# Kernel optimization log

Hardware: AMD Instinct MI355X
Metric: run time of the kernel (lower is better)

## Reference

```python
import jax, jax.numpy as jnp
import numpy as np

B, S, V, E, H, A, L = 64, 256, 32000, 512, 512, 512, 2
EPS = 1e-5


def _ln(x, g, b):
    m = jnp.mean(x, axis=-1, keepdims=True)
    v = jnp.mean((x - m) ** 2, axis=-1, keepdims=True)
    return (x - m) * jax.lax.rsqrt(v + EPS) * g + b


def _lstm_cell(x, h, c, W_ih, W_hh, b_ih, b_hh):
    # torch gate order: i, f, g, o
    gates = x @ W_ih.T + b_ih + h @ W_hh.T + b_hh  # [B, 4H]
    i, f, g, o = jnp.split(gates, 4, axis=-1)
    i, f, o = jax.nn.sigmoid(i), jax.nn.sigmoid(f), jax.nn.sigmoid(o)
    g = jnp.tanh(g)
    c_new = f * c + i * g
    h_new = o * jnp.tanh(c_new)
    return h_new, c_new


def setup_inputs() -> dict:
    key = jax.random.key(0)
    ks = jax.random.split(key, 24)
    d = {}
    d['input_token'] = jax.random.randint(ks[0], (B, 1), 0, V)
    d['h0'] = jax.random.normal(ks[1], (L, B, H), jnp.float32)
    d['c0'] = jax.random.normal(ks[2], (L, B, H), jnp.float32)
    d['encoder_outputs'] = jax.random.normal(ks[3], (B, S, 2 * H), jnp.float32)
    d['encoder_mask'] = jnp.ones((B, S), jnp.int32)
    sc = lambda fi, fo: float(np.sqrt(6.0 / (fi + fo)))
    d['emb'] = jax.random.normal(ks[4], (V, E), jnp.float32) * 0.1
    d['ln_emb_g'] = jnp.ones((E,), jnp.float32)
    d['ln_emb_b'] = jnp.zeros((E,), jnp.float32)
    d['W_enc'] = jax.random.uniform(ks[5], (A, 2 * H), jnp.float32, -sc(2 * H, A), sc(2 * H, A))
    d['b_enc'] = jnp.zeros((A,), jnp.float32)
    d['W_dec'] = jax.random.uniform(ks[6], (A, H), jnp.float32, -sc(H, A), sc(H, A))
    d['b_dec'] = jnp.zeros((A,), jnp.float32)
    d['v_att'] = jax.random.uniform(ks[7], (1, A), jnp.float32, -sc(A, 1), sc(A, 1))
    d['ln_att_g'] = jnp.ones((A,), jnp.float32)
    d['ln_att_b'] = jnp.zeros((A,), jnp.float32)
    in0, in1 = E + 2 * H, H
    d['W_ih0'] = jax.random.uniform(ks[8], (4 * H, in0), jnp.float32, -sc(in0, 4 * H), sc(in0, 4 * H))
    d['W_hh0'] = jax.random.normal(ks[9], (4 * H, H), jnp.float32) * 0.05
    d['b_ih0'] = jnp.zeros((4 * H,), jnp.float32).at[H:2 * H].set(1.0)
    d['b_hh0'] = jnp.zeros((4 * H,), jnp.float32)
    d['W_ih1'] = jax.random.uniform(ks[10], (4 * H, in1), jnp.float32, -sc(in1, 4 * H), sc(in1, 4 * H))
    d['W_hh1'] = jax.random.normal(ks[11], (4 * H, H), jnp.float32) * 0.05
    d['b_ih1'] = jnp.zeros((4 * H,), jnp.float32).at[H:2 * H].set(1.0)
    d['b_hh1'] = jnp.zeros((4 * H,), jnp.float32)
    d['ln_lstm_g'] = jnp.ones((H,), jnp.float32)
    d['ln_lstm_b'] = jnp.zeros((H,), jnp.float32)
    d['W_ctx'] = jax.random.uniform(ks[12], (H, 2 * H), jnp.float32, -sc(2 * H, H), sc(2 * H, H))
    d['b_ctx'] = jnp.zeros((H,), jnp.float32)
    d['W_out'] = jax.random.uniform(ks[13], (V, H), jnp.float32, -sc(H, V), sc(H, V))
    d['b_out'] = jnp.zeros((V,), jnp.float32)
    return d


def reference(input_token, h0, c0, encoder_outputs, encoder_mask,
              emb, ln_emb_g, ln_emb_b,
              W_enc, b_enc, W_dec, b_dec, v_att, ln_att_g, ln_att_b,
              W_ih0, W_hh0, b_ih0, b_hh0, W_ih1, W_hh1, b_ih1, b_hh1,
              ln_lstm_g, ln_lstm_b, W_ctx, b_ctx, W_out, b_out):
    # embedding + norm (dropout = identity in eval)
    embedded = _ln(emb[input_token], ln_emb_g, ln_emb_b)  # [B,1,E]

    # attention using top-layer hidden state
    dec_h = h0[-1]  # [B,H]
    enc_proj = jnp.einsum('bsk,ak->bsa', encoder_outputs, W_enc) + b_enc
    dec_proj = dec_h @ W_dec.T + b_dec  # [B,A]
    combined = _ln(enc_proj + dec_proj[:, None, :], ln_att_g, ln_att_b)
    scores = jnp.einsum('bsa,a->bs', jnp.tanh(combined), v_att[0])
    scores = jnp.where(encoder_mask == 0, -jnp.inf, scores)
    attn_w = jax.nn.softmax(scores, axis=1)  # [B,S]
    context = jnp.einsum('bs,bsk->bk', attn_w, encoder_outputs)  # [B,2H]

    # single-step 2-layer LSTM
    x = jnp.concatenate([embedded[:, 0, :], context], axis=-1)  # [B,E+2H]
    h_l0, c_l0 = _lstm_cell(x, h0[0], c0[0], W_ih0, W_hh0, b_ih0, b_hh0)
    h_l1, c_l1 = _lstm_cell(h_l0, h0[1], c0[1], W_ih1, W_hh1, b_ih1, b_hh1)
    h_new = jnp.stack([h_l0, h_l1])
    c_new = jnp.stack([c_l0, c_l1])

    lstm_out = _ln(h_l1, ln_lstm_g, ln_lstm_b)  # [B,H]
    proj_ctx = context @ W_ctx.T + b_ctx  # [B,H]
    logits = (lstm_out + proj_ctx) @ W_out.T + b_out  # [B,V]
    return logits[:, None, :], (h_new, c_new), attn_w
```

## Files before the change

### kernel.cpp

```cpp
#include <hip/hip_runtime.h>

typedef unsigned int u32;
typedef unsigned short u16;
typedef __attribute__((ext_vector_type(8))) short short8;
typedef __attribute__((ext_vector_type(4))) float f32x4;

__device__ __forceinline__ float bf2f(u16 u) {
  union { u32 i; float f; } v; v.i = ((u32)u) << 16; return v.f;
}
__device__ __forceinline__ u16 f2bf(float f) {
  union { float f; u32 i; } v; v.f = f;
  u32 u = v.i;
  u += 0x7FFFu + ((u >> 16) & 1u);
  return (u16)(u >> 16);
}
__device__ __forceinline__ float tanh_fast(float x) {
  float e = __expf(-2.f * fabsf(x));
  float r = (1.f - e) / (1.f + e);
  return x < 0.f ? -r : r;
}
__device__ __forceinline__ float sigmoid_fast(float x) {
  return 1.f / (1.f + __expf(-x));
}
__device__ __forceinline__ float ld1r(const void* p, size_t i, int f32w) {
  return f32w ? ((const float*)p)[i] : bf2f(((const u16*)p)[i]);
}
__device__ __forceinline__ void outst(void* p, size_t i, float v, int f32o) {
  if (f32o) ((float*)p)[i] = v; else ((u16*)p)[i] = f2bf(v);
}
__device__ __forceinline__ int flag_of(const u32* lnegp) {
  return (lnegp[0] == 0x3F800000u) ? 1 : 0;
}

#define OFF_H    2048000
#define OFF_C    2113536
#define OFF_ATTN 2179072

#define A_LNAG 0
#define A_LNAB 512
#define A_VAT  1024
#define A_BENC 1536
#define A_BDEC 2048
#define A_BIH0 2560
#define A_BHH0 4608
#define A_BIH1 6656
#define A_BHH1 8704
#define A_LNLG 10752
#define A_LNLB 11264
#define A_BCTX 11776
#define A_BOUT 12288
#define A_TOTAL 44288

struct SrcPtrs {
  const void *h0, *c0, *emb, *lneg, *lneb, *Wenc, *benc, *Wdec, *bdec, *vat,
             *lnag, *lnab, *bih0, *bhh0, *bih1, *bhh1, *lnlg, *lnlb, *Wctx,
             *bctx, *bout;
  const int *tok;
};

__device__ __forceinline__ void convblk_r(const void* src, u16* dst, size_t base, int f32w) {
  size_t i0 = base + (size_t)threadIdx.x * 16;
  if (f32w) {
    const float* s = (const float*)src + i0;
    float4 a = *(const float4*)s, b = *(const float4*)(s + 4);
    float4 c = *(const float4*)(s + 8), d = *(const float4*)(s + 12);
    short8 v0, v1;
    v0[0]=(short)f2bf(a.x); v0[1]=(short)f2bf(a.y); v0[2]=(short)f2bf(a.z); v0[3]=(short)f2bf(a.w);
    v0[4]=(short)f2bf(b.x); v0[5]=(short)f2bf(b.y); v0[6]=(short)f2bf(b.z); v0[7]=(short)f2bf(b.w);
    v1[0]=(short)f2bf(c.x); v1[1]=(short)f2bf(c.y); v1[2]=(short)f2bf(c.z); v1[3]=(short)f2bf(c.w);
    v1[4]=(short)f2bf(d.x); v1[5]=(short)f2bf(d.y); v1[6]=(short)f2bf(d.z); v1[7]=(short)f2bf(d.w);
    *(short8*)(dst + i0) = v0; *(short8*)(dst + i0 + 8) = v1;
  } else {
    const uint4* s = (const uint4*)((const u16*)src + i0);
    uint4 a = s[0], b = s[1];
    *(uint4*)(dst + i0) = a; *((uint4*)(dst + i0) + 1) = b;
  }
}

__global__ __launch_bounds__(256) void k_conv(
    const u32* __restrict__ lnegp, SrcPtrs P,
    u16* __restrict__ xcat, u16* __restrict__ xcat1,
    float* __restrict__ c0f, float* __restrict__ arena,
    u16* __restrict__ Wencbf, u16* __restrict__ Wctxbf,
    float* __restrict__ dpf)
{
  const int f32w = flag_of(lnegp);
  __shared__ float red[8];
  __shared__ float hs[512];
  __shared__ float part[256];
  const int t = threadIdx.x;
  const int blk = blockIdx.x;
  if (blk < 64) {
    const int b = blk;
    const int tk = P.tok[b];
    float e0 = ld1r(P.emb, (size_t)tk * 512 + t, f32w);
    float e1 = ld1r(P.emb, (size_t)tk * 512 + t + 256, f32w);
    float s = e0 + e1, ss = e0 * e0 + e1 * e1;
    #pragma unroll
    for (int o = 1; o < 64; o <<= 1) { s += __shfl_xor(s, o, 64); ss += __shfl_xor(ss, o, 64); }
    if ((t & 63) == 0) { red[t >> 6] = s; red[4 + (t >> 6)] = ss; }
    __syncthreads();
    s = red[0] + red[1] + red[2] + red[3];
    ss = red[4] + red[5] + red[6] + red[7];
    const float mean = s * (1.f / 512.f);
    const float rstd = rsqrtf(fmaxf(ss * (1.f / 512.f) - mean * mean, 0.f) + 1e-5f);
    xcat[b*2048 + t]       = f2bf((e0 - mean) * rstd * ld1r(P.lneg, t, f32w) + ld1r(P.lneb, t, f32w));
    xcat[b*2048 + t + 256] = f2bf((e1 - mean) * rstd * ld1r(P.lneg, t + 256, f32w) + ld1r(P.lneb, t + 256, f32w));
    xcat[b*2048 + 1536 + t]       = f2bf(ld1r(P.h0, (size_t)b * 512 + t, f32w));
    xcat[b*2048 + 1536 + t + 256] = f2bf(ld1r(P.h0, (size_t)b * 512 + t + 256, f32w));
  } else if (blk < 128) {
    const int b = blk - 64;
    for (int j = t; j < 512; j += 256) {
      float h1 = ld1r(P.h0, 32768 + (size_t)b * 512 + j, f32w);
      xcat1[b*1024 + 512 + j] = f2bf(h1);
      c0f[b*512 + j]         = ld1r(P.c0, (size_t)b * 512 + j, f32w);
      c0f[32768 + b*512 + j] = ld1r(P.c0, 32768 + (size_t)b * 512 + j, f32w);
    }
  } else if (blk < 256) {
    const int qb = (blk - 128) * 512;
    #pragma unroll
    for (int u = 0; u < 2; u++) {
      int Qi = qb + u * 256 + t;
      int kc = Qi >> 11, rem = Qi & 2047;
      int cq = rem >> 9, col = rem & 511;
      size_t src = (size_t)col * 1024 + kc * 32 + cq * 8;
      if (f32w) {
        const float* s = (const float*)P.Wenc + src;
        float4 a = *(const float4*)s, b2 = *(const float4*)(s + 4);
        short8 v;
        v[0]=(short)f2bf(a.x); v[1]=(short)f2bf(a.y); v[2]=(short)f2bf(a.z); v[3]=(short)f2bf(a.w);
        v[4]=(short)f2bf(b2.x); v[5]=(short)f2bf(b2.y); v[6]=(short)f2bf(b2.z); v[7]=(short)f2bf(b2.w);
        *(short8*)(Wencbf + (size_t)Qi * 8) = v;
      } else {
        *(uint4*)(Wencbf + (size_t)Qi * 8) = *(const uint4*)((const u16*)P.Wenc + src);
      }
    }
  } else if (blk < 384) {
    convblk_r(P.Wctx, Wctxbf, (size_t)(blk - 256) * 4096, f32w);
  } else if (blk < 640) {
    const int db = blk - 384;
    const int b2 = db >> 2, cg = db & 3;
    if (f32w) {
      float2 v = *(const float2*)((const float*)P.h0 + 32768 + (size_t)b2 * 512 + t * 2);
      hs[t * 2] = v.x; hs[t * 2 + 1] = v.y;
    } else {
      u32 u2 = *(const u32*)((const u16*)P.h0 + 32768 + (size_t)b2 * 512 + t * 2);
      hs[t * 2] = bf2f((u16)(u2 & 0xffff)); hs[t * 2 + 1] = bf2f((u16)(u2 >> 16));
    }
    __syncthreads();
    const int col = cg * 128 + (t & 127);
    const int kh = (t >> 7) * 256;
    float acc = 0.f;
    if (f32w) {
      const float* wp = (const float*)P.Wdec + (size_t)col * 512 + kh;
      #pragma unroll 4
      for (int k = 0; k < 256; k += 8) {
        float4 a = *(const float4*)(wp + k), b4 = *(const float4*)(wp + k + 4);
        acc += hs[kh+k]*a.x + hs[kh+k+1]*a.y + hs[kh+k+2]*a.z + hs[kh+k+3]*a.w
             + hs[kh+k+4]*b4.x + hs[kh+k+5]*b4.y + hs[kh+k+6]*b4.z + hs[kh+k+7]*b4.w;
      }
    } else {
      const u16* wp = (const u16*)P.Wdec + (size_t)col * 512 + kh;
      #pragma unroll 4
      for (int k = 0; k < 256; k += 8) {
        short8 wv = *(const short8*)(wp + k);
        #pragma unroll
        for (int i = 0; i < 8; i++) acc += hs[kh + k + i] * bf2f((u16)wv[i]);
      }
    }
    part[t] = acc;
    __syncthreads();
    if (t < 128) {
      float v = part[t] + part[t + 128];
      dpf[b2 * 512 + col] = v + ld1r(P.benc, col, f32w) + ld1r(P.bdec, col, f32w);
    }
  } else {
    int base = (blk - 640) * 4096;
    for (int i = t; i < 4096; i += 256) {
      int v = base + i;
      if (v >= A_TOTAL) break;
      const void* s; int off;
      if      (v < 512)   { s = P.lnag; off = v; }
      else if (v < 1024)  { s = P.lnab; off = v - 512; }
      else if (v < 1536)  { s = P.vat;  off = v - 1024; }
      else if (v < 2048)  { s = P.benc; off = v - 1536; }
      else if (v < 2560)  { s = P.bdec; off = v - 2048; }
      else if (v < 4608)  { s = P.bih0; off = v - 2560; }
      else if (v < 6656)  { s = P.bhh0; off = v - 4608; }
      else if (v < 8704)  { s = P.bih1; off = v - 6656; }
      else if (v < 10752) { s = P.bhh1; off = v - 8704; }
      else if (v < 11264) { s = P.lnlg; off = v - 10752; }
      else if (v < 11776) { s = P.lnlb; off = v - 11264; }
      else if (v < 12288) { s = P.bctx; off = v - 11776; }
      else                { s = P.bout; off = v - 12288; }
      arena[v] = ld1r(s, off, f32w);
    }
  }
}

__global__ __launch_bounds__(512, 4) void k_scores(
    const u32* __restrict__ lnegp,
    const void* __restrict__ enc, const u16* __restrict__ WencT,
    const float* __restrict__ dpf, const float* __restrict__ arena,
    const int* __restrict__ mask, float* __restrict__ scores)
{
  const int f32w = flag_of(lnegp);
  __shared__ __align__(16) char sm[8192];
  const int t = threadIdx.x, wave = t >> 6, lane = t & 63;
  const int q = lane >> 4, r15 = lane & 15;
  const int m0 = blockIdx.x * 32, b = m0 >> 8, n0 = wave * 64;
  const int arow = t >> 2, acq = t & 3;
  const int aslot = ((acq << 5) + (arow ^ (acq << 1))) * 16;

  const u16* bp = WencT + (size_t)((q << 9) + n0 + r15) * 8;
  const float* aF = (const float*)enc + (size_t)(m0 + arow) * 1024 + (acq << 3);
  const u16*   aH = (const u16*)enc   + (size_t)(m0 + arow) * 1024 + (acq << 3);

  short8 Bst[2][4];
  float4 Af[2][2];
  uint4  Au[2];

  auto issueB = [&](int set, int kt) {
    const u16* p = bp + (size_t)kt * 16384;
    Bst[set][0] = *(const short8*)(p);
    Bst[set][1] = *(const short8*)(p + 128);
    Bst[set][2] = *(const short8*)(p + 256);
    Bst[set][3] = *(const short8*)(p + 384);
  };
  auto issueA = [&](int set, int kc) {
    if (f32w) {
      const float* p = aF + kc;
      Af[set][0] = *(const float4*)p;
      Af[set][1] = *(const float4*)(p + 4);
    } else {
      Au[set] = *(const uint4*)(aH + kc);
    }
  };
  auto writeA = [&](int buf, int set) {
    short8 v;
    if (f32w) {
      float4 a = Af[set][0], b2 = Af[set][1];
      v[0]=(short)f2bf(a.x); v[1]=(short)f2bf(a.y); v[2]=(short)f2bf(a.z); v[3]=(short)f2bf(a.w);
      v[4]=(short)f2bf(b2.x); v[5]=(short)f2bf(b2.y); v[6]=(short)f2bf(b2.z); v[7]=(short)f2bf(b2.w);
    } else {
      union { uint4 u; short8 s; } cv; cv.u = Au[set]; v = cv.s;
    }
    *(short8*)(sm + buf * 2048 + aslot) = v;
  };

  if (t < 128) { issueA(1, 0); issueA(0, 32); }
  issueB(0, 0);
  if (t < 128) writeA(0, 1);
  __builtin_amdgcn_sched_barrier(0);
  asm volatile("s_waitcnt lgkmcnt(0)" ::: "memory");
  __builtin_amdgcn_s_barrier();
  __builtin_amdgcn_sched_barrier(0);

  f32x4 acc[2][4] = {};
  #pragma unroll 2
  for (int kt = 0; kt < 32; ++kt) {
    const int cur = kt & 1, nxt = cur ^ 1;
    if (t < 128) issueA(nxt, ((kt + 2 < 32) ? (kt + 2) : 31) << 5);
    issueB(nxt, (kt + 1 < 32) ? (kt + 1) : 31);
    short8 af[2];
    #pragma unroll
    for (int mi = 0; mi < 2; mi++) {
      int slot = (q << 5) + ((mi * 16 + r15) ^ (q << 1));
      af[mi] = *(const short8*)(sm + cur * 2048 + slot * 16);
    }
    #pragma unroll
    for (int mi = 0; mi < 2; mi++)
      #pragma unroll
      for (int ni = 0; ni < 4; ni++)
        acc[mi][ni] = __builtin_amdgcn_mfma_f32_16x16x32_bf16(af[mi], Bst[cur][ni], acc[mi][ni], 0, 0, 0);
    if (t < 128 && kt + 1 < 32) writeA(nxt, cur);
    __builtin_amdgcn_sched_barrier(0);
    asm volatile("s_waitcnt lgkmcnt(0)" ::: "memory");
    __builtin_amdgcn_s_barrier();
    __builtin_amdgcn_sched_barrier(0);
  }

  float dpv[4];
  #pragma unroll
  for (int ni = 0; ni < 4; ni++)
    dpv[ni] = dpf[b * 512 + n0 + ni * 16 + r15];

  float* ps    = (float*)(sm + 4096);
  float* pq    = (float*)(sm + 5120);
  float* mean_ = (float*)(sm + 6144);
  float* rstd_ = (float*)(sm + 6272);
  #pragma unroll
  for (int mi = 0; mi < 2; mi++)
    #pragma unroll
    for (int r = 0; r < 4; r++) {
      float s = 0.f, sq = 0.f;
      #pragma unroll
      for (int ni = 0; ni < 4; ni++) {
        float x = acc[mi][ni][r] + dpv[ni];
        s += x; sq += x * x;
      }
      #pragma unroll
      for (int o = 1; o < 16; o <<= 1) { s += __shfl_xor(s, o, 64); sq += __shfl_xor(sq, o, 64); }
      if (r15 == 0) { int row = mi*16 + q*4 + r; ps[wave*32 + row] = s; pq[wave*32 + row] = sq; }
    }
  __syncthreads();
  if (t < 32) {
    float s = 0.f, sq = 0.f;
    #pragma unroll
    for (int w = 0; w < 8; w++) { s += ps[w*32 + t]; sq += pq[w*32 + t]; }
    float mn = s * (1.f / 512.f);
    mean_[t] = mn;
    rstd_[t] = rsqrtf(fmaxf(sq * (1.f / 512.f) - mn * mn, 0.f) + 1e-5f);
  }
  __syncthreads();
  float g4[4], b4[4], v4[4];
  #pragma unroll
  for (int ni = 0; ni < 4; ni++) {
    int col = n0 + ni*16 + r15;
    g4[ni] = arena[A_LNAG + col]; b4[ni] = arena[A_LNAB + col]; v4[ni] = arena[A_VAT + col];
  }
  #pragma unroll
  for (int mi = 0; mi < 2; mi++)
    #pragma unroll
    for (int r = 0; r < 4; r++) {
      int row = mi*16 + q*4 + r;
      float mn = mean_[row], rs = rstd_[row];
      float s = 0.f;
      #pragma unroll
      for (int ni = 0; ni < 4; ni++) {
        float x = acc[mi][ni][r] + dpv[ni];
        float y = (x - mn) * rs * g4[ni] + b4[ni];
        s += tanh_fast(y) * v4[ni];
      }
      #pragma unroll
      for (int o = 1; o < 16; o <<= 1) s += __shfl_xor(s, o, 64);
      if (r15 == 0) ps[wave*32 + row] = s;
    }
  __syncthreads();
  if (t < 32) {
    float sc = 0.f;
    #pragma unroll
    for (int w = 0; w < 8; w++) sc += ps[w*32 + t];
    int s_ = (m0 & 255) + t;
    scores[m0 + t] = mask[b*256 + s_] ? sc : -__builtin_inff();
  }
}

__global__ __launch_bounds__(256) void k_softmax_ctx(
    const u32* __restrict__ lnegp,
    const float* __restrict__ scores, const void* __restrict__ enc,
    u16* __restrict__ xcat, void* __restrict__ out)
{
  const int f32w = flag_of(lnegp);
  __shared__ float aw[256];
  __shared__ float red[8];
  __shared__ float px[1024];
  const int t = threadIdx.x;
  const int b = blockIdx.x >> 2, kq = blockIdx.x & 3;
  float sv = scores[b * 256 + t];
  float mx = sv;
  #pragma unroll
  for (int o = 1; o < 64; o <<= 1) mx = fmaxf(mx, __shfl_xor(mx, o, 64));
  if ((t & 63) == 0) red[t >> 6] = mx;
  __syncthreads();
  mx = fmaxf(fmaxf(red[0], red[1]), fmaxf(red[2], red[3]));
  float e = __expf(sv - mx);
  float s = e;
  #pragma unroll
  for (int o = 1; o < 64; o <<= 1) s += __shfl_xor(s, o, 64);
  if ((t & 63) == 0) red[4 + (t >> 6)] = s;
  __syncthreads();
  s = red[4] + red[5] + red[6] + red[7];
  float w = e / s;
  aw[t] = w;
  if (kq == 0) outst(out, OFF_ATTN + b * 256 + t, w, f32w);
  __syncthreads();
  const int kk = t & 63, sg = t >> 6;
  float a0 = 0.f, a1 = 0.f, a2 = 0.f, a3 = 0.f;
  if (f32w) {
    const float* p = (const float*)enc + (size_t)b * 262144 + kq * 256 + kk * 4;
    #pragma unroll 8
    for (int i = 0; i < 64; i++) {
      int si = i * 4 + sg;
      float4 v = *(const float4*)(p + (size_t)si * 1024);
      float w_ = aw[si];
      a0 += w_ * v.x; a1 += w_ * v.y; a2 += w_ * v.z; a3 += w_ * v.w;
    }
  } else {
    const u16* p = (const u16*)enc + (size_t)b * 262144 + kq * 256 + kk * 4;
    #pragma unroll 8
    for (int i = 0; i < 64; i++) {
      int si = i * 4 + sg;
      uint2 u = *(const uint2*)(p + (size_t)si * 1024);
      float w_ = aw[si];
      a0 += w_ * bf2f((u16)(u.x & 0xffff)); a1 += w_ * bf2f((u16)(u.x >> 16));
      a2 += w_ * bf2f((u16)(u.y & 0xffff)); a3 += w_ * bf2f((u16)(u.y >> 16));
    }
  }
  px[sg * 256 + kk * 4]     = a0;
  px[sg * 256 + kk * 4 + 1] = a1;
  px[sg * 256 + kk * 4 + 2] = a2;
  px[sg * 256 + kk * 4 + 3] = a3;
  __syncthreads();
  float cv = px[t] + px[256 + t] + px[512 + t] + px[768 + t];
  xcat[b * 2048 + 512 + kq * 256 + t] = f2bf(cv);
}

__global__ __launch_bounds__(512) void k_lstm(
    const u32* __restrict__ lnegp,
    const u16* __restrict__ x, int K,
    const void* __restrict__ Wa, int Ka,
    const void* __restrict__ Wb, int Kb,
    int boff_ih, int boff_hh,
    const float* __restrict__ arena, const float* __restrict__ c0f, int coff,
    void* __restrict__ out, size_t h_off, size_t c_off,
    u16* __restrict__ aux_bf, float* __restrict__ aux_f)
{
  const int f32w = flag_of(lnegp);
  __shared__ __align__(16) char sm[24576];
  const int t = threadIdx.x, wave = t >> 6, lane = t & 63;
  const int q = lane >> 4, r15 = lane & 15;
  const int jt = blockIdx.x & 127, bh = blockIdx.x >> 7;
  const int kslice = K >> 3, ksteps = kslice >> 5;
  const int k0 = wave * kslice;
  const void* W; int Kw, koff;
  if (k0 < Ka) { W = Wa; Kw = Ka; koff = k0; }
  else         { W = Wb; Kw = Kb; koff = k0 - Ka; }
  char* slab = sm + wave * 3072;
  const int bc = lane >> 2, bcq = lane & 3;
  const int wrow = (bc >> 2) * 512 + jt * 4 + (bc & 3);
  f32x4 acc4[2] = {};

  for (int st = 0; st < ksteps; ++st) {
    const int kA = k0 + st * 32;
    const int kB = koff + st * 32;
    #pragma unroll
    for (int i = 0; i < 2; i++) {
      int id = i * 64 + lane;
      int row = id >> 2, cq = id & 3;
      *(uint4*)(slab + (cq * 32 + row) * 16) =
          *(const uint4*)(x + (size_t)(bh * 32 + row) * K + kA + cq * 8);
    }
    {
      size_t wi = (size_t)wrow * Kw + kB + bcq * 8;
      short8 bv;
      if (f32w) {
        const float* wp = (const float*)W + wi;
        float4 a = *(const float4*)wp, b = *(const float4*)(wp + 4);
        bv[0]=(short)f2bf(a.x); bv[1]=(short)f2bf(a.y); bv[2]=(short)f2bf(a.z); bv[3]=(short)f2bf(a.w);
        bv[4]=(short)f2bf(b.x); bv[5]=(short)f2bf(b.y); bv[6]=(short)f2bf(b.z); bv[7]=(short)f2bf(b.w);
      } else {
        bv = *(const short8*)((const u16*)W + wi);
      }
      *(short8*)(slab + 2048 + (bcq * 16 + bc) * 16) = bv;
    }
    short8 af[2];
    #pragma unroll
    for (int mi = 0; mi < 2; mi++)
      af[mi] = *(const short8*)(slab + (q * 32 + mi * 16 + r15) * 16);
    short8 bfrg = *(const short8*)(slab + 2048 + (q * 16 + r15) * 16);
    #pragma unroll
    for (int mi = 0; mi < 2; mi++)
      acc4[mi] = __builtin_amdgcn_mfma_f32_16x16x32_bf16(af[mi], bfrg, acc4[mi], 0, 0, 0);
  }
  __syncthreads();
  float* part = (float*)sm;
  #pragma unroll
  for (int mi = 0; mi < 2; mi++)
    #pragma unroll
    for (int r = 0; r < 4; r++)
      part[wave * 512 + (mi * 16 + q * 4 + r) * 16 + r15] = acc4[mi][r];
  __syncthreads();
  if (t < 128) {
    const int b_ = t >> 2, cl = t & 3;
    const int bg = bh * 32 + b_;
    const int jg = jt * 4 + cl;
    float g4[4];
    #pragma unroll
    for (int g = 0; g < 4; g++) {
      float v = 0.f;
      #pragma unroll
      for (int w = 0; w < 8; w++) v += part[w * 512 + b_ * 16 + g * 4 + cl];
      g4[g] = v + arena[boff_ih + g * 512 + jg] + arena[boff_hh + g * 512 + jg];
    }
    float i_ = sigmoid_fast(g4[0]), f_ = sigmoid_fast(g4[1]), o_ = sigmoid_fast(g4[3]);
    float gg = tanh_fast(g4[2]);
    float c_ = f_ * c0f[coff + bg * 512 + jg] + i_ * gg;
    float h_ = o_ * tanh_fast(c_);
    outst(out, h_off + bg * 512 + jg, h_, f32w);
    outst(out, c_off + bg * 512 + jg, c_, f32w);
    if (aux_bf) aux_bf[bg * 1024 + jg] = f2bf(h_);
    if (aux_f)  aux_f[bg * 512 + jg] = h_;
  }
}

__global__ __launch_bounds__(256) void k_svec(
    const float* __restrict__ hl1f, const u16* __restrict__ xcat,
    const u16* __restrict__ Wctxbf, const float* __restrict__ arena,
    u16* __restrict__ svec)
{
  __shared__ float ctx[1024];
  __shared__ float red[8];
  const int t = threadIdx.x, b = blockIdx.x >> 1, hf = blockIdx.x & 1;
  for (int i = t; i < 1024; i += 256) ctx[i] = bf2f(xcat[b * 2048 + 512 + i]);
  float h0v = hl1f[b * 512 + t], h1v = hl1f[b * 512 + t + 256];
  float s = h0v + h1v, ss = h0v * h0v + h1v * h1v;
  #pragma unroll
  for (int o = 1; o < 64; o <<= 1) { s += __shfl_xor(s, o, 64); ss += __shfl_xor(ss, o, 64); }
  if ((t & 63) == 0) { red[t >> 6] = s; red[4 + (t >> 6)] = ss; }
  __syncthreads();
  s = red[0] + red[1] + red[2] + red[3];
  ss = red[4] + red[5] + red[6] + red[7];
  const float mean = s * (1.f / 512.f);
  const float rstd = rsqrtf(fmaxf(ss * (1.f / 512.f) - mean * mean, 0.f) + 1e-5f);
  const int hh = hf * 256 + t;
  float hv = hl1f[b * 512 + hh];
  float lnv = (hv - mean) * rstd * arena[A_LNLG + hh] + arena[A_LNLB + hh];
  float acc = arena[A_BCTX + hh];
  #pragma unroll 4
  for (int k = 0; k < 1024; k += 8) {
    short8 wv = *(const short8*)(Wctxbf + (size_t)hh * 1024 + k);
    #pragma unroll
    for (int i = 0; i < 8; i++) acc += ctx[k + i] * bf2f((u16)wv[i]);
  }
  svec[b * 512 + hh] = f2bf(lnv + acc);
}

__global__ __launch_bounds__(256) void k_logits(
    const u32* __restrict__ lnegp,
    const u16* __restrict__ svec, const void* __restrict__ Wout,
    const float* __restrict__ arena, void* __restrict__ out)
{
  const int f32w = flag_of(lnegp);
  const int t = threadIdx.x, wave = t >> 6, lane = t & 63;
  const int q = lane >> 4, r15 = lane & 15;
  const int col = blockIdx.x * 64 + wave * 16 + r15;
  const float* wF = (const float*)Wout + (size_t)col * 512 + (q << 3);
  const u16*   wH = (const u16*)Wout   + (size_t)col * 512 + (q << 3);
  const u16*   sv = svec + (size_t)r15 * 512 + (q << 3);
  f32x4 acc[4] = {};
  #pragma unroll 4
  for (int kc = 0; kc < 16; ++kc) {
    short8 bfr;
    if (f32w) {
      float4 a = *(const float4*)(wF + (kc << 5));
      float4 b2 = *(const float4*)(wF + (kc << 5) + 4);
      bfr[0]=(short)f2bf(a.x); bfr[1]=(short)f2bf(a.y); bfr[2]=(short)f2bf(a.z); bfr[3]=(short)f2bf(a.w);
      bfr[4]=(short)f2bf(b2.x); bfr[5]=(short)f2bf(b2.y); bfr[6]=(short)f2bf(b2.z); bfr[7]=(short)f2bf(b2.w);
    } else {
      bfr = *(const short8*)(wH + (kc << 5));
    }
    #pragma unroll
    for (int mi = 0; mi < 4; mi++) {
      short8 af = *(const short8*)(sv + (size_t)(mi * 16) * 512 + (kc << 5));
      acc[mi] = __builtin_amdgcn_mfma_f32_16x16x32_bf16(af, bfr, acc[mi], 0, 0, 0);
    }
  }
  float bo = arena[A_BOUT + col];
  #pragma unroll
  for (int mi = 0; mi < 4; mi++)
    #pragma unroll
    for (int r = 0; r < 4; r++) {
      int brow = mi * 16 + q * 4 + r;
      outst(out, (size_t)brow * 32000 + col, acc[mi][r] + bo, f32w);
    }
}

extern "C" void kernel_launch(void* const* d_in, const int* in_sizes, int n_in,
                              void* d_out, int out_size, void* d_ws, size_t ws_size,
                              hipStream_t stream)
{
  SrcPtrs P;
  P.tok  = (const int*)d_in[0];
  P.h0   = d_in[1];  P.c0   = d_in[2];
  const void* enc = d_in[3];
  const int* mask = (const int*)d_in[4];
  P.emb  = d_in[5]; P.lneg = d_in[6]; P.lneb = d_in[7];
  P.Wenc = d_in[8]; P.benc = d_in[9]; P.Wdec = d_in[10]; P.bdec = d_in[11];
  P.vat  = d_in[12]; P.lnag = d_in[13]; P.lnab = d_in[14];
  P.bih0 = d_in[17]; P.bhh0 = d_in[18];
  P.bih1 = d_in[21]; P.bhh1 = d_in[22];
  P.lnlg = d_in[23]; P.lnlb = d_in[24];
  P.Wctx = d_in[25]; P.bctx = d_in[26];
  const void* Wout = d_in[27];
  P.bout = d_in[28];
  const void* Wih0 = d_in[15];
  const void* Whh0 = d_in[16];
  const void* Wih1 = d_in[19];
  const void* Whh1 = d_in[20];
  const u32* lnegp = (const u32*)P.lneg;

  char* ws = (char*)d_ws;
  float* arena   = (float*)(ws + 256);
  u16*   Wencbf  = (u16*)(ws + 177664);
  u16*   Wctxbf  = (u16*)(ws + 1750528);
  u16*   xcat    = (u16*)(ws + 2799104);
  u16*   xcat1   = (u16*)(ws + 3061248);
  float* c0f     = (float*)(ws + 3257856);
  float* scores  = (float*)(ws + 3520000);
  float* hl1f    = (float*)(ws + 3585536);
  u16*   svec    = (u16*)(ws + 3716608);
  float* dpf     = (float*)(ws + 3782144);

  k_conv<<<651, 256, 0, stream>>>(lnegp, P, xcat, xcat1, c0f, arena, Wencbf, Wctxbf, dpf);
  k_scores<<<512, 512, 0, stream>>>(lnegp, enc, Wencbf, dpf, arena, mask, scores);
  k_softmax_ctx<<<256, 256, 0, stream>>>(lnegp, scores, enc, xcat, d_out);
  k_lstm<<<256, 512, 0, stream>>>(lnegp, xcat, 2048, Wih0, 1536, Whh0, 512,
                                  A_BIH0, A_BHH0, arena, c0f, 0,
                                  d_out, OFF_H, OFF_C, xcat1, (float*)nullptr);
  k_lstm<<<256, 512, 0, stream>>>(lnegp, xcat1, 1024, Wih1, 512, Whh1, 512,
                                  A_BIH1, A_BHH1, arena, c0f, 32768,
                                  d_out, OFF_H + 32768, OFF_C + 32768,
                                  (u16*)nullptr, hl1f);
  k_svec<<<128, 256, 0, stream>>>(hl1f, xcat, Wctxbf, arena, svec);
  k_logits<<<500, 256, 0, stream>>>(lnegp, svec, Wout, arena, d_out);
}
```

Baseline: 358.8 us.

## Load encoder A-fragments directly to registers and widen softmax-context blocks

The scores GEMM now has every wave load its own A fragments from global memory straight into registers, converting them with packed bf16 conversion instructions. This removes the shared-memory staging and the per-iteration block barriers. It also staggers each block's starting K tile to spread memory traffic. The softmax/context kernel doubles its threads to 512 so each thread handles half as many sequence rows, reducing per-thread loop length. The trade-off is redundant global A loads across the 8 waves (relying on cache) and more register use.

Result: slower. 550.2 us (+53.4%).

```diff
diff --git a/kernel.cpp b/kernel.cpp
--- a/kernel.cpp
+++ b/kernel.cpp
@@ -13,6 +13,11 @@
   u32 u = v.i;
   u += 0x7FFFu + ((u >> 16) & 1u);
   return (u16)(u >> 16);
+}
+__device__ __forceinline__ u32 cvtpk(float lo, float hi) {
+  u32 r;
+  asm("v_cvt_pk_bf16_f32 %0, %1, %2" : "=v"(r) : "v"(lo), "v"(hi));
+  return r;
 }
 __device__ __forceinline__ float tanh_fast(float x) {
   float e = __expf(-2.f * fabsf(x));
@@ -205,20 +210,22 @@
     const int* __restrict__ mask, float* __restrict__ scores)
 {
   const int f32w = flag_of(lnegp);
-  __shared__ __align__(16) char sm[8192];
+  __shared__ float eps[256];
+  __shared__ float epq[256];
+  __shared__ float emean[32];
+  __shared__ float erstd[32];
   const int t = threadIdx.x, wave = t >> 6, lane = t & 63;
   const int q = lane >> 4, r15 = lane & 15;
   const int m0 = blockIdx.x * 32, b = m0 >> 8, n0 = wave * 64;
-  const int arow = t >> 2, acq = t & 3;
-  const int aslot = ((acq << 5) + (arow ^ (acq << 1))) * 16;
 
   const u16* bp = WencT + (size_t)((q << 9) + n0 + r15) * 8;
-  const float* aF = (const float*)enc + (size_t)(m0 + arow) * 1024 + (acq << 3);
-  const u16*   aH = (const u16*)enc   + (size_t)(m0 + arow) * 1024 + (acq << 3);
+  const float* aF0 = (const float*)enc + (size_t)(m0 + r15) * 1024 + (q << 3);
+  const float* aF1 = aF0 + 16 * 1024;
+  const u16*   aH0 = (const u16*)enc + (size_t)(m0 + r15) * 1024 + (q << 3);
+  const u16*   aH1 = aH0 + 16 * 1024;
 
   short8 Bst[2][4];
-  float4 Af[2][2];
-  uint4  Au[2];
+  uint4 Ar[2][2][2];
 
   auto issueB = [&](int set, int kt) {
     const u16* p = bp + (size_t)kt * 16384;
@@ -227,57 +234,52 @@
     Bst[set][2] = *(const short8*)(p + 256);
     Bst[set][3] = *(const short8*)(p + 384);
   };
-  auto issueA = [&](int set, int kc) {
+  auto issueA = [&](int set, int kt) {
     if (f32w) {
-      const float* p = aF + kc;
-      Af[set][0] = *(const float4*)p;
-      Af[set][1] = *(const float4*)(p + 4);
+      const float* p0 = aF0 + (kt << 5);
+      const float* p1 = aF1 + (kt << 5);
+      Ar[set][0][0] = *(const uint4*)(p0);
+      Ar[set][0][1] = *(const uint4*)(p0 + 4);
+      Ar[set][1][0] = *(const uint4*)(p1);
+      Ar[set][1][1] = *(const uint4*)(p1 + 4);
     } else {
-      Au[set] = *(const uint4*)(aH + kc);
+      Ar[set][0][0] = *(const uint4*)(aH0 + (kt << 5));
+      Ar[set][1][0] = *(const uint4*)(aH1 + (kt << 5));
     }
   };
-  auto writeA = [&](int buf, int set) {
-    short8 v;
+  auto mkA = [&](int set, int frag) -> short8 {
+    union { u32 w[4]; short8 s; uint4 u4; } u;
     if (f32w) {
-      float4 a = Af[set][0], b2 = Af[set][1];
-      v[0]=(short)f2bf(a.x); v[1]=(short)f2bf(a.y); v[2]=(short)f2bf(a.z); v[3]=(short)f2bf(a.w);
-      v[4]=(short)f2bf(b2.x); v[5]=(short)f2bf(b2.y); v[6]=(short)f2bf(b2.z); v[7]=(short)f2bf(b2.w);
+      const float* f0 = (const float*)&Ar[set][frag][0];
+      const float* f1 = (const float*)&Ar[set][frag][1];
+      u.w[0] = cvtpk(f0[0], f0[1]);
+      u.w[1] = cvtpk(f0[2], f0[3]);
+      u.w[2] = cvtpk(f1[0], f1[1]);
+      u.w[3] = cvtpk(f1[2], f1[3]);
     } else {
-      union { uint4 u; short8 s; } cv; cv.u = Au[set]; v = cv.s;
-    }
-    *(short8*)(sm + buf * 2048 + aslot) = v;
+      u.u4 = Ar[set][frag][0];
+    }
+    return u.s;
   };
 
-  if (t < 128) { issueA(1, 0); issueA(0, 32); }
-  issueB(0, 0);
-  if (t < 128) writeA(0, 1);
-  __builtin_amdgcn_sched_barrier(0);
-  asm volatile("s_waitcnt lgkmcnt(0)" ::: "memory");
-  __builtin_amdgcn_s_barrier();
-  __builtin_amdgcn_sched_barrier(0);
-
+  const int kstart = blockIdx.x & 31;
+  issueB(0, kstart);
+  issueA(0, kstart);
   f32x4 acc[2][4] = {};
   #pragma unroll 2
-  for (int kt = 0; kt < 32; ++kt) {
-    const int cur = kt & 1, nxt = cur ^ 1;
-    if (t < 128) issueA(nxt, ((kt + 2 < 32) ? (kt + 2) : 31) << 5);
-    issueB(nxt, (kt + 1 < 32) ? (kt + 1) : 31);
-    short8 af[2];
-    #pragma unroll
-    for (int mi = 0; mi < 2; mi++) {
-      int slot = (q << 5) + ((mi * 16 + r15) ^ (q << 1));
-      af[mi] = *(const short8*)(sm + cur * 2048 + slot * 16);
-    }
-    #pragma unroll
-    for (int mi = 0; mi < 2; mi++)
-      #pragma unroll
-      for (int ni = 0; ni < 4; ni++)
-        acc[mi][ni] = __builtin_amdgcn_mfma_f32_16x16x32_bf16(af[mi], Bst[cur][ni], acc[mi][ni], 0, 0, 0);
-    if (t < 128 && kt + 1 < 32) writeA(nxt, cur);
-    __builtin_amdgcn_sched_barrier(0);
-    asm volatile("s_waitcnt lgkmcnt(0)" ::: "memory");
-    __builtin_amdgcn_s_barrier();
-    __builtin_amdgcn_sched_barrier(0);
+  for (int i = 0; i < 32; ++i) {
+    const int cur = i & 1, nxt = cur ^ 1;
+    if (i + 1 < 32) {
+      int ktn = (kstart + i + 1) & 31;
+      issueB(nxt, ktn);
+      issueA(nxt, ktn);
+    }
+    short8 a0 = mkA(cur, 0), a1 = mkA(cur, 1);
+    #pragma unroll
+    for (int ni = 0; ni < 4; ni++) {
+      acc[0][ni] = __builtin_amdgcn_mfma_f32_16x16x32_bf16(a0, Bst[cur][ni], acc[0][ni], 0, 0, 0);
+      acc[1][ni] = __builtin_amdgcn_mfma_f32_16x16x32_bf16(a1, Bst[cur][ni], acc[1][ni], 0, 0, 0);
+    }
   }
 
   float dpv[4];
@@ -285,10 +287,6 @@
   for (int ni = 0; ni < 4; ni++)
     dpv[ni] = dpf[b * 512 + n0 + ni * 16 + r15];
 
-  float* ps    = (float*)(sm + 4096);
-  float* pq    = (float*)(sm + 5120);
-  float* mean_ = (float*)(sm + 6144);
-  float* rstd_ = (float*)(sm + 6272);
   #pragma unroll
   for (int mi = 0; mi < 2; mi++)
     #pragma unroll
@@ -301,16 +299,16 @@
       }
       #pragma unroll
       for (int o = 1; o < 16; o <<= 1) { s += __shfl_xor(s, o, 64); sq += __shfl_xor(sq, o, 64); }
-      if (r15 == 0) { int row = mi*16 + q*4 + r; ps[wave*32 + row] = s; pq[wave*32 + row] = sq; }
+      if (r15 == 0) { int row = mi*16 + q*4 + r; eps[wave*32 + row] = s; epq[wave*32 + row] = sq; }
     }
   __syncthreads();
   if (t < 32) {
     float s = 0.f, sq = 0.f;
     #pragma unroll
-    for (int w = 0; w < 8; w++) { s += ps[w*32 + t]; sq += pq[w*32 + t]; }
+    for (int w = 0; w < 8; w++) { s += eps[w*32 + t]; sq += epq[w*32 + t]; }
     float mn = s * (1.f / 512.f);
-    mean_[t] = mn;
-    rstd_[t] = rsqrtf(fmaxf(sq * (1.f / 512.f) - mn * mn, 0.f) + 1e-5f);
+    emean[t] = mn;
+    erstd[t] = rsqrtf(fmaxf(sq * (1.f / 512.f) - mn * mn, 0.f) + 1e-5f);
   }
   __syncthreads();
   float g4[4], b4[4], v4[4];
@@ -324,7 +322,7 @@
     #pragma unroll
     for (int r = 0; r < 4; r++) {
       int row = mi*16 + q*4 + r;
-      float mn = mean_[row], rs = rstd_[row];
+      float mn = emean[row], rs = erstd[row];
       float s = 0.f;
       #pragma unroll
       for (int ni = 0; ni < 4; ni++) {
@@ -334,54 +332,58 @@
       }
       #pragma unroll
       for (int o = 1; o < 16; o <<= 1) s += __shfl_xor(s, o, 64);
-      if (r15 == 0) ps[wave*32 + row] = s;
+      if (r15 == 0) eps[wave*32 + row] = s;
     }
   __syncthreads();
   if (t < 32) {
     float sc = 0.f;
     #pragma unroll
-    for (int w = 0; w < 8; w++) sc += ps[w*32 + t];
+    for (int w = 0; w < 8; w++) sc += eps[w*32 + t];
     int s_ = (m0 & 255) + t;
     scores[m0 + t] = mask[b*256 + s_] ? sc : -__builtin_inff();
   }
 }
 
-__global__ __launch_bounds__(256) void k_softmax_ctx(
+__global__ __launch_bounds__(512) void k_softmax_ctx(
     const u32* __restrict__ lnegp,
     const float* __restrict__ scores, const void* __restrict__ enc,
     u16* __restrict__ xcat, void* __restrict__ out)
 {
   const int f32w = flag_of(lnegp);
   __shared__ float aw[256];
-  __shared__ float red[8];
-  __shared__ float px[1024];
+  __shared__ float red[16];
+  __shared__ float px[2048];
   const int t = threadIdx.x;
   const int b = blockIdx.x >> 2, kq = blockIdx.x & 3;
-  float sv = scores[b * 256 + t];
-  float mx = sv;
-  #pragma unroll
-  for (int o = 1; o < 64; o <<= 1) mx = fmaxf(mx, __shfl_xor(mx, o, 64));
-  if ((t & 63) == 0) red[t >> 6] = mx;
-  __syncthreads();
-  mx = fmaxf(fmaxf(red[0], red[1]), fmaxf(red[2], red[3]));
-  float e = __expf(sv - mx);
-  float s = e;
-  #pragma unroll
-  for (int o = 1; o < 64; o <<= 1) s += __shfl_xor(s, o, 64);
-  if ((t & 63) == 0) red[4 + (t >> 6)] = s;
-  __syncthreads();
-  s = red[4] + red[5] + red[6] + red[7];
-  float w = e / s;
-  aw[t] = w;
-  if (kq == 0) outst(out, OFF_ATTN + b * 256 + t, w, f32w);
+  {
+    float sv = (t < 256) ? scores[b * 256 + t] : -__builtin_inff();
+    float mx = sv;
+    #pragma unroll
+    for (int o = 1; o < 64; o <<= 1) mx = fmaxf(mx, __shfl_xor(mx, o, 64));
+    if ((t & 63) == 0) red[t >> 6] = mx;
+    __syncthreads();
+    mx = fmaxf(fmaxf(red[0], red[1]), fmaxf(red[2], red[3]));
+    float e = __expf(sv - mx);
+    float s = e;
+    #pragma unroll
+    for (int o = 1; o < 64; o <<= 1) s += __shfl_xor(s, o, 64);
+    if ((t & 63) == 0) red[8 + (t >> 6)] = s;
+    __syncthreads();
+    s = red[8] + red[9] + red[10] + red[11];
+    if (t < 256) {
+      float w = e / s;
+      aw[t] = w;
+      if (kq == 0) outst(out, OFF_ATTN + b * 256 + t, w, f32w);
+    }
+  }
   __syncthreads();
   const int kk = t & 63, sg = t >> 6;
   float a0 = 0.f, a1 = 0.f, a2 = 0.f, a3 = 0.f;
   if (f32w) {
     const float* p = (const float*)enc + (size_t)b * 262144 + kq * 256 + kk * 4;
     #pragma unroll 8
-    for (int i = 0; i < 64; i++) {
-      int si = i * 4 + sg;
+    for (int i = 0; i < 32; i++) {
+      int si = i * 8 + sg;
       float4 v = *(const float4*)(p + (size_t)si * 1024);
       float w_ = aw[si];
       a0 += w_ * v.x; a1 += w_ * v.y; a2 += w_ * v.z; a3 += w_ * v.w;
@@ -389,8 +391,8 @@
   } else {
     const u16* p = (const u16*)enc + (size_t)b * 262144 + kq * 256 + kk * 4;
     #pragma unroll 8
-    for (int i = 0; i < 64; i++) {
-      int si = i * 4 + sg;
+    for (int i = 0; i < 32; i++) {
+      int si = i * 8 + sg;
       uint2 u = *(const uint2*)(p + (size_t)si * 1024);
       float w_ = aw[si];
       a0 += w_ * bf2f((u16)(u.x & 0xffff)); a1 += w_ * bf2f((u16)(u.x >> 16));
@@ -402,8 +404,12 @@
   px[sg * 256 + kk * 4 + 2] = a2;
   px[sg * 256 + kk * 4 + 3] = a3;
   __syncthreads();
-  float cv = px[t] + px[256 + t] + px[512 + t] + px[768 + t];
-  xcat[b * 2048 + 512 + kq * 256 + t] = f2bf(cv);
+  if (t < 256) {
+    float cv = 0.f;
+    #pragma unroll
+    for (int g = 0; g < 8; g++) cv += px[g * 256 + t];
+    xcat[b * 2048 + 512 + kq * 256 + t] = f2bf(cv);
+  }
 }
 
 __global__ __launch_bounds__(512) void k_lstm(
@@ -604,7 +610,7 @@
 
   k_conv<<<651, 256, 0, stream>>>(lnegp, P, xcat, xcat1, c0f, arena, Wencbf, Wctxbf, dpf);
   k_scores<<<512, 512, 0, stream>>>(lnegp, enc, Wencbf, dpf, arena, mask, scores);
-  k_softmax_ctx<<<256, 256, 0, stream>>>(lnegp, scores, enc, xcat, d_out);
+  k_softmax_ctx<<<256, 512, 0, stream>>>(lnegp, scores, enc, xcat, d_out);
   k_lstm<<<256, 512, 0, stream>>>(lnegp, xcat, 2048, Wih0, 1536, Whh0, 512,
                                   A_BIH0, A_BHH0, arena, c0f, 0,
                                   d_out, OFF_H, OFF_C, xcat1, (float*)nullptr);
```
